# Kernel tuning notes

Hardware: AMD Instinct MI355X
Metric: run time of the kernel (lower is better)

## Reference

```python
import jax, jax.numpy as jnp
import numpy as np
import math

BATCH, SEQ, D_MODEL, HEADS = 2, 2048, 1024, 16
DK = D_MODEL // HEADS  # 64
THETA = 10000.0


def _init_linear(key, d_in, d_out):
    std = math.sqrt(2.0 / (d_in + d_out))
    return (jax.random.truncated_normal(key, -3.0, 3.0, (d_in, d_out), jnp.float32) * std)


def setup_inputs() -> dict:
    key = jax.random.key(0)
    kx, kq, kk, kv, ko = jax.random.split(key, 5)
    x = jax.random.normal(kx, (BATCH, SEQ, D_MODEL), jnp.float32)
    W_Q = _init_linear(kq, D_MODEL, D_MODEL)
    W_K = _init_linear(kk, D_MODEL, D_MODEL)
    W_V = _init_linear(kv, D_MODEL, D_MODEL)
    W_O = _init_linear(ko, D_MODEL, D_MODEL)
    token_positions = jnp.arange(SEQ, dtype=jnp.int64 if jax.config.jax_enable_x64 else jnp.int32)
    # RoPE tables: angle[i, k] = i / theta**(2k/d_k), shape [max_seq_len, d_k//2]
    pos = jnp.arange(SEQ, dtype=jnp.float32)[:, None]
    inv_freq = THETA ** (-2.0 * jnp.arange(DK // 2, dtype=jnp.float32) / DK)
    angles = pos * inv_freq
    return {
        "x": x,
        "token_positions": token_positions,
        "W_Q": W_Q,
        "W_K": W_K,
        "W_V": W_V,
        "W_O": W_O,
        "cos": jnp.cos(angles),
        "sin": jnp.sin(angles),
    }


def _apply_rope(t, cos_p, sin_p):
    # t: [B, H, S, DK]; cos_p/sin_p: [S, DK//2] (already gathered by position)
    t_even = t[..., 0::2]
    t_odd = t[..., 1::2]
    even_rot = cos_p * t_even - sin_p * t_odd
    odd_rot = sin_p * t_even + cos_p * t_odd
    # interleave back: [..., DK//2, 2] -> [..., DK]
    return jnp.stack([even_rot, odd_rot], axis=-1).reshape(t.shape)


def reference(x, token_positions, W_Q, W_K, W_V, W_O, cos, sin):
    B, S, D = x.shape
    H, dk = HEADS, D // HEADS
    # QKV projections, split into heads: [B, S, D] -> [B, H, S, dk]
    def proj(W):
        return jnp.einsum("bsd,de->bse", x, W).reshape(B, S, H, dk).transpose(0, 2, 1, 3)
    Q, K, V = proj(W_Q), proj(W_K), proj(W_V)
    cos_p = cos[token_positions]  # [S, dk//2]
    sin_p = sin[token_positions]
    Q = _apply_rope(Q, cos_p, sin_p)
    K = _apply_rope(K, cos_p, sin_p)
    scores = jnp.einsum("bhqd,bhkd->bhqk", Q, K) / jnp.sqrt(jnp.asarray(dk, x.dtype))
    causal = jnp.tril(jnp.ones((S, S), dtype=bool))
    scores = jnp.where(causal, scores, -jnp.inf)
    attn = jax.nn.softmax(scores, axis=-1)
    out = jnp.einsum("bhqk,bhkd->bhqd", attn, V)  # [B, H, S, dk]
    out = out.transpose(0, 2, 1, 3).reshape(B, S, D)
    return jnp.einsum("bsd,de->bse", out, W_O)
```

## Files before the change

kernel.cpp:

```cpp
#include <hip/hip_runtime.h>

typedef unsigned short u16;
typedef unsigned int   u32;
typedef __bf16  bf16x8 __attribute__((ext_vector_type(8)));
typedef float   f32x4  __attribute__((ext_vector_type(4)));
typedef u32     u32x4  __attribute__((ext_vector_type(4)));

#define SEQ    2048
#define HEADS  16
#define DM     1024
#define NBH    32
#define NBS    4096

#define LOG2E  1.4426950408889634f

__device__ __forceinline__ u16 f2b(float f) {
    u32 x;
    __builtin_memcpy(&x, &f, 4);
    return (u16)((x + 0x7fffu + ((x >> 16) & 1u)) >> 16);
}

__device__ __forceinline__ u32 pkc(float lo, float hi) {
    __bf16 a = (__bf16)lo, b = (__bf16)hi;
    u16 x, y;
    __builtin_memcpy(&x, &a, 2);
    __builtin_memcpy(&y, &b, 2);
    return (u32)x | ((u32)y << 16);
}

__device__ __forceinline__ bf16x8 ld_bf8(const u16* p) {
    return *(const bf16x8*)p;
}

__device__ __forceinline__ void gl_lds16(const u16* g, __bf16* l) {
    __builtin_amdgcn_global_load_lds(
        (__attribute__((address_space(1))) void*)g,
        (__attribute__((address_space(3))) void*)l,
        16, 0, 0);
}

__global__ __launch_bounds__(256) void transpose_wqkv(const float* __restrict__ Wq,
                                                      const float* __restrict__ Wk,
                                                      const float* __restrict__ Wv,
                                                      u16* __restrict__ WqkvT) {
    __shared__ u16 tile[64][65];
    const int z  = blockIdx.z;
    const float* src = (z == 0) ? Wq : (z == 1) ? Wk : Wv;
    const int k0 = blockIdx.x * 64, n0 = blockIdx.y * 64;
    const int tid = threadIdx.x;
    for (int i = 0; i < 16; ++i) {
        int e = i * 256 + tid;
        int r = e >> 6, c = e & 63;
        tile[r][c] = f2b(src[(size_t)(k0 + r) * DM + n0 + c]);
    }
    __syncthreads();
    u16* dst = WqkvT + (size_t)z * DM * DM;
    for (int i = 0; i < 16; ++i) {
        int e = i * 256 + tid;
        int r = e >> 6, c = e & 63;
        dst[(size_t)(n0 + r) * DM + k0 + c] = tile[c][r];
    }
}

__global__ __launch_bounds__(256) void transpose_wo(const float* __restrict__ Wo,
                                                    u16* __restrict__ WoT) {
    __shared__ u16 tile[64][65];
    const int k0 = blockIdx.x * 64, n0 = blockIdx.y * 64;
    const int tid = threadIdx.x;
    for (int i = 0; i < 16; ++i) {
        int e = i * 256 + tid;
        int r = e >> 6, c = e & 63;
        tile[r][c] = f2b(Wo[(size_t)(k0 + r) * DM + n0 + c]);
    }
    __syncthreads();
    for (int i = 0; i < 16; ++i) {
        int e = i * 256 + tid;
        int r = e >> 6, c = e & 63;
        WoT[(size_t)(n0 + r) * DM + k0 + c] = tile[c][r];
    }
}

__global__ __launch_bounds__(256) void cvt_x(const float* __restrict__ x,
                                             u16* __restrict__ xb) {
    int t = blockIdx.x * 256 + threadIdx.x;
    const float* p = x + (size_t)t * 8;
    f32x4 a = *(const f32x4*)p;
    f32x4 b = *(const f32x4*)(p + 4);
    u32x4 v;
    v[0] = pkc(a[0], a[1]);
    v[1] = pkc(a[2], a[3]);
    v[2] = pkc(b[0], b[1]);
    v[3] = pkc(b[2], b[3]);
    *(u32x4*)(xb + (size_t)t * 8) = v;
}

__global__ __launch_bounds__(256) void gemm_qkv(const u16* __restrict__ Ab,
                                                const u16* __restrict__ Bt,
                                                u16* __restrict__ Qp,
                                                u16* __restrict__ Kp,
                                                u16* __restrict__ Vt) {
    __shared__ __attribute__((aligned(16))) __bf16 As[128 * 64];
    __shared__ __attribute__((aligned(16))) __bf16 Bs[128 * 64];
    const int tid  = threadIdx.x;
    const int wave = tid >> 6, lane = tid & 63;
    const int quad = lane >> 4, col = lane & 15;
    const int wm = wave >> 1, wn = wave & 1;
    const int m0 = blockIdx.x * 128, n0 = blockIdx.y * 128;
    const int srow = tid >> 3;
    const int aslot = (((tid & 7) ^ (srow & 7)) << 3);
    const int c7 = col & 7;

    f32x4 zero = {0.f, 0.f, 0.f, 0.f};
    f32x4 acc[4][4];
    for (int i = 0; i < 4; ++i)
        for (int j = 0; j < 4; ++j) acc[i][j] = zero;

    for (int k0 = 0; k0 < DM; k0 += 64) {
        __syncthreads();
#pragma unroll
        for (int p = 0; p < 4; ++p)
            gl_lds16(Ab + (size_t)(m0 + p * 32 + srow) * DM + k0 + aslot,
                     &As[p * 2048 + tid * 8]);
#pragma unroll
        for (int p = 0; p < 4; ++p)
            gl_lds16(Bt + (size_t)(n0 + p * 32 + srow) * DM + k0 + aslot,
                     &Bs[p * 2048 + tid * 8]);
        __syncthreads();
#pragma unroll
        for (int ks = 0; ks < 2; ++ks) {
            const int rsl = ((((ks << 2) | quad) ^ c7) << 3);
            bf16x8 af[4], bfr[4];
#pragma unroll
            for (int mt = 0; mt < 4; ++mt)
                af[mt] = *(const bf16x8*)&As[(wm * 64 + mt * 16 + col) * 64 + rsl];
#pragma unroll
            for (int nt = 0; nt < 4; ++nt)
                bfr[nt] = *(const bf16x8*)&Bs[(wn * 64 + nt * 16 + col) * 64 + rsl];
#pragma unroll
            for (int mt = 0; mt < 4; ++mt)
#pragma unroll
                for (int nt = 0; nt < 4; ++nt)
                    acc[mt][nt] = __builtin_amdgcn_mfma_f32_16x16x32_bf16(
                        af[mt], bfr[nt], acc[mt][nt], 0, 0, 0);
        }
    }

    for (int mt = 0; mt < 4; ++mt)
        for (int nt = 0; nt < 4; ++nt) {
            int cc = n0 + wn * 64 + nt * 16 + col;
            int which = cc >> 10;
            int c1 = cc & 1023;
            int h = c1 >> 6, d = c1 & 63;
            for (int r = 0; r < 4; ++r) {
                int row = m0 + wm * 64 + mt * 16 + quad * 4 + r;
                int b = row >> 11, s = row & (SEQ - 1);
                u16 val = f2b(acc[mt][nt][r]);
                size_t bh = (size_t)(b * HEADS + h);
                if (which == 0)
                    Qp[(bh * SEQ + s) * 64 + d] = val;
                else if (which == 1)
                    Kp[(bh * SEQ + s) * 64 + d] = val;
                else
                    Vt[(bh * 64 + d) * SEQ + s] = val;
            }
        }
}

__global__ __launch_bounds__(256) void gemm_wo(const u16* __restrict__ A,
                                               const u16* __restrict__ Bt,
                                               float* __restrict__ C) {
    __shared__ __attribute__((aligned(16))) __bf16 As[128 * 64];
    __shared__ __attribute__((aligned(16))) __bf16 Bs[64 * 64];
    const int tid  = threadIdx.x;
    const int wave = tid >> 6, lane = tid & 63;
    const int quad = lane >> 4, col = lane & 15;
    const int m0 = blockIdx.x * 128, n0 = blockIdx.y * 64;
    const int srow = tid >> 3;
    const int aslot = (((tid & 7) ^ (srow & 7)) << 3);
    const int c7 = col & 7;

    f32x4 zero = {0.f, 0.f, 0.f, 0.f};
    f32x4 acc[2][4];
    for (int i = 0; i < 2; ++i)
        for (int j = 0; j < 4; ++j) acc[i][j] = zero;

    for (int k0 = 0; k0 < DM; k0 += 64) {
        __syncthreads();
#pragma unroll
        for (int p = 0; p < 4; ++p)
            gl_lds16(A + (size_t)(m0 + p * 32 + srow) * DM + k0 + aslot,
                     &As[p * 2048 + tid * 8]);
#pragma unroll
        for (int p = 0; p < 2; ++p)
            gl_lds16(Bt + (size_t)(n0 + p * 32 + srow) * DM + k0 + aslot,
                     &Bs[p * 2048 + tid * 8]);
        __syncthreads();
#pragma unroll
        for (int ks = 0; ks < 2; ++ks) {
            const int rsl = ((((ks << 2) | quad) ^ c7) << 3);
            bf16x8 af[2], bfr[4];
#pragma unroll
            for (int mt = 0; mt < 2; ++mt)
                af[mt] = *(const bf16x8*)&As[(wave * 32 + mt * 16 + col) * 64 + rsl];
#pragma unroll
            for (int nt = 0; nt < 4; ++nt)
                bfr[nt] = *(const bf16x8*)&Bs[(nt * 16 + col) * 64 + rsl];
#pragma unroll
            for (int mt = 0; mt < 2; ++mt)
#pragma unroll
                for (int nt = 0; nt < 4; ++nt)
                    acc[mt][nt] = __builtin_amdgcn_mfma_f32_16x16x32_bf16(
                        af[mt], bfr[nt], acc[mt][nt], 0, 0, 0);
        }
    }

    for (int mt = 0; mt < 2; ++mt)
        for (int nt = 0; nt < 4; ++nt)
            for (int r = 0; r < 4; ++r) {
                int row = m0 + wave * 32 + mt * 16 + quad * 4 + r;
                int cc  = n0 + nt * 16 + col;
                C[(size_t)row * DM + cc] = acc[mt][nt][r];
            }
}

__global__ __launch_bounds__(256) void rope_qk(u16* __restrict__ Qp,
                                               u16* __restrict__ Kp,
                                               const float* __restrict__ cosT,
                                               const float* __restrict__ sinT) {
    int t = blockIdx.x * 256 + threadIdx.x;
    int g  = t & 7;
    int s  = (t >> 3) & (SEQ - 1);
    int hh = (t >> 14) & (HEADS - 1);
    int b  = t >> 18;

    f32x4 cv = *(const f32x4*)&cosT[s * 32 + g * 4];
    f32x4 sv = *(const f32x4*)&sinT[s * 32 + g * 4];

    const float QS = 0.125f * LOG2E;
    size_t addr = (((size_t)(b * HEADS + hh)) * SEQ + s) * 64 + g * 8;
    u32x4 q4 = *(const u32x4*)(Qp + addr);
    u32x4 k4 = *(const u32x4*)(Kp + addr);
    u32x4 qo4, ko4;
#pragma unroll
    for (int j = 0; j < 4; ++j) {
        u32 q2 = q4[j], k2 = k4[j];
        u32 qe_b = (q2 & 0xffff) << 16, qo_b = q2 & 0xffff0000u;
        u32 ke_b = (k2 & 0xffff) << 16, ko_b = k2 & 0xffff0000u;
        float qe, qo, ke, ko;
        __builtin_memcpy(&qe, &qe_b, 4); __builtin_memcpy(&qo, &qo_b, 4);
        __builtin_memcpy(&ke, &ke_b, 4); __builtin_memcpy(&ko, &ko_b, 4);
        qo4[j] = (u32)f2b(QS * (cv[j] * qe - sv[j] * qo)) |
                 ((u32)f2b(QS * (sv[j] * qe + cv[j] * qo)) << 16);
        ko4[j] = (u32)f2b(cv[j] * ke - sv[j] * ko) |
                 ((u32)f2b(sv[j] * ke + cv[j] * ko) << 16);
    }
    *(u32x4*)(Qp + addr) = qo4;
    *(u32x4*)(Kp + addr) = ko4;
}

__global__ __launch_bounds__(64) void flash_attn(const u16* __restrict__ Qp,
                                                 const u16* __restrict__ Kp,
                                                 const u16* __restrict__ Vt,
                                                 u16* __restrict__ O) {
    const int lane = threadIdx.x;
    const int quad = lane >> 4, col = lane & 15;
    const bool hi5 = lane >= 32;
    const bool hi4 = (lane & 16) != 0;
    const int bh = blockIdx.x;
    const int b = bh >> 4, h = bh & 15;
    const int qt = 63 - blockIdx.y;
    const int q0 = qt * 32;

    const u16* Qb = Qp + (size_t)bh * SEQ * 64;
    const u16* Kb = Kp + (size_t)bh * SEQ * 64;
    const u16* Vb = Vt + (size_t)bh * 64 * SEQ;

    bf16x8 bq00 = ld_bf8(Qb + (size_t)(q0 + col) * 64 + quad * 8);
    bf16x8 bq01 = ld_bf8(Qb + (size_t)(q0 + col) * 64 + 32 + quad * 8);
    bf16x8 bq10 = ld_bf8(Qb + (size_t)(q0 + 16 + col) * 64 + quad * 8);
    bf16x8 bq11 = ld_bf8(Qb + (size_t)(q0 + 16 + col) * 64 + 32 + quad * 8);

    f32x4 zero = {0.f, 0.f, 0.f, 0.f};
    f32x4 o0[4] = {zero, zero, zero, zero};
    f32x4 o1[4] = {zero, zero, zero, zero};
    float m0_ = -1e30f, m1_ = -1e30f;
    float lp0 = 0.f, lp1 = 0.f;

    const int nkt = qt + 1;

    bf16x8 ck00 = ld_bf8(Kb + (size_t)col * 64 + quad * 8);
    bf16x8 ck01 = ld_bf8(Kb + (size_t)col * 64 + 32 + quad * 8);
    bf16x8 ck10 = ld_bf8(Kb + (size_t)(16 + col) * 64 + quad * 8);
    bf16x8 ck11 = ld_bf8(Kb + (size_t)(16 + col) * 64 + 32 + quad * 8);
    bf16x8 cv0  = ld_bf8(Vb + (size_t)(0 * 16 + col) * SEQ + quad * 8);
    bf16x8 cv1  = ld_bf8(Vb + (size_t)(1 * 16 + col) * SEQ + quad * 8);
    bf16x8 cv2  = ld_bf8(Vb + (size_t)(2 * 16 + col) * SEQ + quad * 8);
    bf16x8 cv3  = ld_bf8(Vb + (size_t)(3 * 16 + col) * SEQ + quad * 8);

    for (int kt = 0; kt < nkt; ++kt) {
        const int kb = kt << 5;
        const int kb2 = kb + 32;
        bf16x8 nk00 = ld_bf8(Kb + (size_t)(kb2 + col) * 64 + quad * 8);
        bf16x8 nk01 = ld_bf8(Kb + (size_t)(kb2 + col) * 64 + 32 + quad * 8);
        bf16x8 nk10 = ld_bf8(Kb + (size_t)(kb2 + 16 + col) * 64 + quad * 8);
        bf16x8 nk11 = ld_bf8(Kb + (size_t)(kb2 + 16 + col) * 64 + 32 + quad * 8);
        bf16x8 nv0  = ld_bf8(Vb + (size_t)(0 * 16 + col) * SEQ + kb2 + quad * 8);
        bf16x8 nv1  = ld_bf8(Vb + (size_t)(1 * 16 + col) * SEQ + kb2 + quad * 8);
        bf16x8 nv2  = ld_bf8(Vb + (size_t)(2 * 16 + col) * SEQ + kb2 + quad * 8);
        bf16x8 nv3  = ld_bf8(Vb + (size_t)(3 * 16 + col) * SEQ + kb2 + quad * 8);

        f32x4 s00 = zero, s01 = zero, s10 = zero, s11 = zero;
        s00 = __builtin_amdgcn_mfma_f32_16x16x32_bf16(ck00, bq00, s00, 0, 0, 0);
        s10 = __builtin_amdgcn_mfma_f32_16x16x32_bf16(ck00, bq10, s10, 0, 0, 0);
        s00 = __builtin_amdgcn_mfma_f32_16x16x32_bf16(ck01, bq01, s00, 0, 0, 0);
        s10 = __builtin_amdgcn_mfma_f32_16x16x32_bf16(ck01, bq11, s10, 0, 0, 0);
        s01 = __builtin_amdgcn_mfma_f32_16x16x32_bf16(ck10, bq00, s01, 0, 0, 0);
        s11 = __builtin_amdgcn_mfma_f32_16x16x32_bf16(ck10, bq10, s11, 0, 0, 0);
        s01 = __builtin_amdgcn_mfma_f32_16x16x32_bf16(ck11, bq01, s01, 0, 0, 0);
        s11 = __builtin_amdgcn_mfma_f32_16x16x32_bf16(ck11, bq11, s11, 0, 0, 0);

        float v00[4], v01[4], v10[4], v11[4];
        float lm0 = -1e30f, lm1 = -1e30f;
        if (kt == qt) {
            for (int r = 0; r < 4; ++r) {
                int krel = quad * 4 + r;
                float a0 = (krel > col) ? -1e30f : s00[r];
                float b0 = -1e30f;
                float a1 = s10[r];
                float b1 = (krel > col) ? -1e30f : s11[r];
                v00[r] = a0; v01[r] = b0; v10[r] = a1; v11[r] = b1;
                lm0 = fmaxf(lm0, fmaxf(a0, b0));
                lm1 = fmaxf(lm1, fmaxf(a1, b1));
            }
        } else {
            for (int r = 0; r < 4; ++r) {
                v00[r] = s00[r]; v01[r] = s01[r];
                v10[r] = s10[r]; v11[r] = s11[r];
                lm0 = fmaxf(lm0, fmaxf(v00[r], v01[r]));
                lm1 = fmaxf(lm1, fmaxf(v10[r], v11[r]));
            }
        }

        float dd = fmaxf(lm0 - m0_, lm1 - m1_);
        if (__any(dd > 11.54f)) {
            float lr0 = fmaxf(lm0, __shfl_xor(lm0, 16));
            lr0 = fmaxf(lr0, __shfl_xor(lr0, 32));
            float lr1 = fmaxf(lm1, __shfl_xor(lm1, 16));
            lr1 = fmaxf(lr1, __shfl_xor(lr1, 32));
            float mn0 = fmaxf(m0_, lr0), mn1 = fmaxf(m1_, lr1);
            float al0 = __builtin_amdgcn_exp2f(m0_ - mn0);
            float al1 = __builtin_amdgcn_exp2f(m1_ - mn1);
            m0_ = mn0; m1_ = mn1;
            lp0 *= al0; lp1 *= al1;
            for (int r = 0; r < 4; ++r) {
                float ar0 = __shfl(al0, quad * 4 + r);
                float ar1 = __shfl(al1, quad * 4 + r);
                for (int nt = 0; nt < 4; ++nt) {
                    o0[nt][r] *= ar0;
                    o1[nt][r] *= ar1;
                }
            }
        }

        for (int r = 0; r < 4; ++r) {
            v00[r] = __builtin_amdgcn_exp2f(v00[r] - m0_);
            v01[r] = __builtin_amdgcn_exp2f(v01[r] - m0_);
            v10[r] = __builtin_amdgcn_exp2f(v10[r] - m1_);
            v11[r] = __builtin_amdgcn_exp2f(v11[r] - m1_);
            lp0 += v00[r] + v01[r];
            lp1 += v10[r] + v11[r];
        }

        u32 fwa0[4], fwa1[4];
        {
            u32 A0 = pkc(v00[0], v00[1]), A1 = pkc(v00[2], v00[3]);
            u32 B0 = pkc(v01[0], v01[1]), B1 = pkc(v01[2], v01[3]);
            u32 g0 = hi5 ? A0 : B0,  g1 = hi5 ? A1 : B1;
            u32 r0 = __shfl_xor(g0, 32), r1 = __shfl_xor(g1, 32);
            u32 P00 = hi5 ? r0 : A0,  P01 = hi5 ? r1 : A1;
            u32 P10 = hi5 ? B0 : r0,  P11 = hi5 ? B1 : r1;
            u32 h0 = hi4 ? P00 : P10, h1 = hi4 ? P01 : P11;
            u32 u0 = __shfl_xor(h0, 16), u1 = __shfl_xor(h1, 16);
            fwa0[0] = hi4 ? u0 : P00;  fwa0[1] = hi4 ? u1 : P01;
            fwa0[2] = hi4 ? P10 : u0;  fwa0[3] = hi4 ? P11 : u1;
        }
        {
            u32 A0 = pkc(v10[0], v10[1]), A1 = pkc(v10[2], v10[3]);
            u32 B0 = pkc(v11[0], v11[1]), B1 = pkc(v11[2], v11[3]);
            u32 g0 = hi5 ? A0 : B0,  g1 = hi5 ? A1 : B1;
            u32 r0 = __shfl_xor(g0, 32), r1 = __shfl_xor(g1, 32);
            u32 P00 = hi5 ? r0 : A0,  P01 = hi5 ? r1 : A1;
            u32 P10 = hi5 ? B0 : r0,  P11 = hi5 ? B1 : r1;
            u32 h0 = hi4 ? P00 : P10, h1 = hi4 ? P01 : P11;
            u32 u0 = __shfl_xor(h0, 16), u1 = __shfl_xor(h1, 16);
            fwa1[0] = hi4 ? u0 : P00;  fwa1[1] = hi4 ? u1 : P01;
            fwa1[2] = hi4 ? P10 : u0;  fwa1[3] = hi4 ? P11 : u1;
        }
        bf16x8 pf0, pf1;
        __builtin_memcpy(&pf0, fwa0, 16);
        __builtin_memcpy(&pf1, fwa1, 16);

        o0[0] = __builtin_amdgcn_mfma_f32_16x16x32_bf16(pf0, cv0, o0[0], 0, 0, 0);
        o1[0] = __builtin_amdgcn_mfma_f32_16x16x32_bf16(pf1, cv0, o1[0], 0, 0, 0);
        o0[1] = __builtin_amdgcn_mfma_f32_16x16x32_bf16(pf0, cv1, o0[1], 0, 0, 0);
        o1[1] = __builtin_amdgcn_mfma_f32_16x16x32_bf16(pf1, cv1, o1[1], 0, 0, 0);
        o0[2] = __builtin_amdgcn_mfma_f32_16x16x32_bf16(pf0, cv2, o0[2], 0, 0, 0);
        o1[2] = __builtin_amdgcn_mfma_f32_16x16x32_bf16(pf1, cv2, o1[2], 0, 0, 0);
        o0[3] = __builtin_amdgcn_mfma_f32_16x16x32_bf16(pf0, cv3, o0[3], 0, 0, 0);
        o1[3] = __builtin_amdgcn_mfma_f32_16x16x32_bf16(pf1, cv3, o1[3], 0, 0, 0);

        ck00 = nk00; ck01 = nk01; ck10 = nk10; ck11 = nk11;
        cv0 = nv0; cv1 = nv1; cv2 = nv2; cv3 = nv3;
    }

    float lt0 = lp0;
    lt0 += __shfl_xor(lt0, 16); lt0 += __shfl_xor(lt0, 32);
    float lt1 = lp1;
    lt1 += __shfl_xor(lt1, 16); lt1 += __shfl_xor(lt1, 32);
    float linv0 = 1.f / lt0;
    float linv1 = 1.f / lt1;
    for (int r = 0; r < 4; ++r) {
        float l0r = __shfl(linv0, quad * 4 + r);
        float l1r = __shfl(linv1, quad * 4 + r);
        int qrA = q0 + quad * 4 + r;
        int qrB = qrA + 16;
        for (int nt = 0; nt < 4; ++nt) {
            O[((size_t)b * SEQ + qrA) * DM + h * 64 + nt * 16 + col] =
                f2b(o0[nt][r] * l0r);
            O[((size_t)b * SEQ + qrB) * DM + h * 64 + nt * 16 + col] =
                f2b(o1[nt][r] * l1r);
        }
    }
}

extern "C" void kernel_launch(void* const* d_in, const int* in_sizes, int n_in,
                              void* d_out, int out_size, void* d_ws, size_t ws_size,
                              hipStream_t stream) {
    const float* x    = (const float*)d_in[0];
    const float* Wq   = (const float*)d_in[2];
    const float* Wk   = (const float*)d_in[3];
    const float* Wv   = (const float*)d_in[4];
    const float* Wo   = (const float*)d_in[5];
    const float* cosT = (const float*)d_in[6];
    const float* sinT = (const float*)d_in[7];
    float* out = (float*)d_out;

    u16* ws    = (u16*)d_ws;
    u16* qp    = ws;
    u16* kp    = ws + 4194304;
    u16* vt    = ws + 8388608;
    u16* woT   = ws + 8388608;
    u16* wqkvT = ws + 12582912;
    u16* ao    = ws + 12582912;
    u16* xb    = (u16*)out;

    dim3 blk(256);
    transpose_wqkv<<<dim3(16, 16, 3), blk, 0, stream>>>(Wq, Wk, Wv, wqkvT);
    cvt_x<<<dim3(2048), blk, 0, stream>>>(x, xb);
    gemm_qkv<<<dim3(32, 24), blk, 0, stream>>>(xb, wqkvT, qp, kp, vt);
    rope_qk<<<dim3(2048), blk, 0, stream>>>(qp, kp, cosT, sinT);
    flash_attn<<<dim3(NBH, 64), dim3(64), 0, stream>>>(qp, kp, vt, ao);
    transpose_wo<<<dim3(16, 16), blk, 0, stream>>>(Wo, woT);
    gemm_wo<<<dim3(32, 16), blk, 0, stream>>>(ao, woT, out);
}
```

Measured before the change: 238.0 us.

## Split causal KV loop across two waves per block and merge via LDS

The flash attention block grows from one wave to two. Each wave handles alternating 32-key tiles and keeps its own running max, sum and output. At the end, wave 1 writes its partial state to shared memory and wave 0 rescales and combines the two before writing the output. The loop now keeps two tiles of K/V in flight per wave, aiming to shorten each block's serial chain and hide more memory and exp latency. The cost is extra shared memory, a block-level barrier, a merge step and more registers per wave.

```diff
diff --git a/kernel.cpp b/kernel.cpp
--- a/kernel.cpp
+++ b/kernel.cpp
@@ -258,11 +258,118 @@
     *(u32x4*)(Kp + addr) = ko4;
 }
 
-__global__ __launch_bounds__(64) void flash_attn(const u16* __restrict__ Qp,
-                                                 const u16* __restrict__ Kp,
-                                                 const u16* __restrict__ Vt,
-                                                 u16* __restrict__ O) {
-    const int lane = threadIdx.x;
+#define FA_MFMA(A, B, C) __builtin_amdgcn_mfma_f32_16x16x32_bf16(A, B, C, 0, 0, 0)
+
+#define FA_LD(K00, K01, K10, K11, V0, V1, V2, V3, T) do {                      \
+    size_t kk_ = (size_t)(T) * 2048;                                           \
+    size_t vv_ = (size_t)(T) * 32;                                             \
+    K00 = ld_bf8(Kb + kk_ + koff);                                             \
+    K01 = ld_bf8(Kb + kk_ + koff + 32);                                        \
+    K10 = ld_bf8(Kb + kk_ + koff + 1024);                                      \
+    K11 = ld_bf8(Kb + kk_ + koff + 1056);                                      \
+    V0  = ld_bf8(Vb + vv_ + voff);                                             \
+    V1  = ld_bf8(Vb + vv_ + voff + 16 * SEQ);                                  \
+    V2  = ld_bf8(Vb + vv_ + voff + 32 * SEQ);                                  \
+    V3  = ld_bf8(Vb + vv_ + voff + 48 * SEQ);                                  \
+} while (0)
+
+#define FA_TILE(K00, K01, K10, K11, V0, V1, V2, V3, KT) do {                   \
+    f32x4 s00 = zero, s01 = zero, s10 = zero, s11 = zero;                      \
+    s00 = FA_MFMA(K00, bq00, s00);  s10 = FA_MFMA(K00, bq10, s10);             \
+    s00 = FA_MFMA(K01, bq01, s00);  s10 = FA_MFMA(K01, bq11, s10);             \
+    s01 = FA_MFMA(K10, bq00, s01);  s11 = FA_MFMA(K10, bq10, s11);             \
+    s01 = FA_MFMA(K11, bq01, s01);  s11 = FA_MFMA(K11, bq11, s11);             \
+    float v00[4], v01[4], v10[4], v11[4];                                      \
+    float lm0 = -1e30f, lm1 = -1e30f;                                          \
+    if ((KT) == qt) {                        \
+        for (int r = 0; r < 4; ++r) {                                          \
+            int krel = quad * 4 + r;                                           \
+            float a0 = (krel > col) ? -1e30f : s00[r];                         \
+            float b0 = -1e30f;                                                 \
+            float a1 = s10[r];                                                 \
+            float b1 = (krel > col) ? -1e30f : s11[r];                         \
+            v00[r] = a0; v01[r] = b0; v10[r] = a1; v11[r] = b1;                \
+            lm0 = fmaxf(lm0, fmaxf(a0, b0));                                   \
+            lm1 = fmaxf(lm1, fmaxf(a1, b1));                                   \
+        }                                                                      \
+    } else {                                                                   \
+        for (int r = 0; r < 4; ++r) {                                          \
+            v00[r] = s00[r]; v01[r] = s01[r];                                  \
+            v10[r] = s10[r]; v11[r] = s11[r];                                  \
+            lm0 = fmaxf(lm0, fmaxf(v00[r], v01[r]));                           \
+            lm1 = fmaxf(lm1, fmaxf(v10[r], v11[r]));                           \
+        }                                                                      \
+    }                                                                          \
+    float dd = fmaxf(lm0 - m0_, lm1 - m1_);                                    \
+    if (__any(dd > 11.54f)) {                     \
+        float lr0 = fmaxf(lm0, __shfl_xor(lm0, 16));                           \
+        lr0 = fmaxf(lr0, __shfl_xor(lr0, 32));                                 \
+        float lr1 = fmaxf(lm1, __shfl_xor(lm1, 16));                           \
+        lr1 = fmaxf(lr1, __shfl_xor(lr1, 32));                                 \
+        float mn0 = fmaxf(m0_, lr0), mn1 = fmaxf(m1_, lr1);                    \
+        float al0 = __builtin_amdgcn_exp2f(m0_ - mn0);                         \
+        float al1 = __builtin_amdgcn_exp2f(m1_ - mn1);                         \
+        m0_ = mn0; m1_ = mn1;                                                  \
+        lp0 *= al0; lp1 *= al1;                                                \
+        for (int r = 0; r < 4; ++r) {                                          \
+            float ar0 = __shfl(al0, quad * 4 + r);                             \
+            float ar1 = __shfl(al1, quad * 4 + r);                             \
+            for (int nt = 0; nt < 4; ++nt) {                                   \
+                o0[nt][r] *= ar0;                                              \
+                o1[nt][r] *= ar1;                                              \
+            }                                                                  \
+        }                                                                      \
+    }                                                                          \
+    for (int r = 0; r < 4; ++r) {                                              \
+        v00[r] = __builtin_amdgcn_exp2f(v00[r] - m0_);                         \
+        v01[r] = __builtin_amdgcn_exp2f(v01[r] - m0_);                         \
+        v10[r] = __builtin_amdgcn_exp2f(v10[r] - m1_);                         \
+        v11[r] = __builtin_amdgcn_exp2f(v11[r] - m1_);                         \
+        lp0 += v00[r] + v01[r];                                                \
+        lp1 += v10[r] + v11[r];                                                \
+    }                                                                          \
+    u32 fwa0[4], fwa1[4];                                                      \
+    {                                                                          \
+        u32 A0 = pkc(v00[0], v00[1]), A1 = pkc(v00[2], v00[3]);                \
+        u32 B0 = pkc(v01[0], v01[1]), B1 = pkc(v01[2], v01[3]);                \
+        u32 g0 = hi5 ? A0 : B0,  g1 = hi5 ? A1 : B1;                           \
+        u32 r0 = __shfl_xor(g0, 32), r1 = __shfl_xor(g1, 32);                  \
+        u32 P00 = hi5 ? r0 : A0,  P01 = hi5 ? r1 : A1;                         \
+        u32 P10 = hi5 ? B0 : r0,  P11 = hi5 ? B1 : r1;                         \
+        u32 h0 = hi4 ? P00 : P10, h1 = hi4 ? P01 : P11;                        \
+        u32 u0 = __shfl_xor(h0, 16), u1 = __shfl_xor(h1, 16);                  \
+        fwa0[0] = hi4 ? u0 : P00;  fwa0[1] = hi4 ? u1 : P01;                   \
+        fwa0[2] = hi4 ? P10 : u0;  fwa0[3] = hi4 ? P11 : u1;                   \
+    }                                                                          \
+    {                                                                          \
+        u32 A0 = pkc(v10[0], v10[1]), A1 = pkc(v10[2], v10[3]);                \
+        u32 B0 = pkc(v11[0], v11[1]), B1 = pkc(v11[2], v11[3]);                \
+        u32 g0 = hi5 ? A0 : B0,  g1 = hi5 ? A1 : B1;                           \
+        u32 r0 = __shfl_xor(g0, 32), r1 = __shfl_xor(g1, 32);                  \
+        u32 P00 = hi5 ? r0 : A0,  P01 = hi5 ? r1 : A1;                         \
+        u32 P10 = hi5 ? B0 : r0,  P11 = hi5 ? B1 : r1;                         \
+        u32 h0 = hi4 ? P00 : P10, h1 = hi4 ? P01 : P11;                        \
+        u32 u0 = __shfl_xor(h0, 16), u1 = __shfl_xor(h1, 16);                  \
+        fwa1[0] = hi4 ? u0 : P00;  fwa1[1] = hi4 ? u1 : P01;                   \
+        fwa1[2] = hi4 ? P10 : u0;  fwa1[3] = hi4 ? P11 : u1;                   \
+    }                                                                          \
+    bf16x8 pf0, pf1;                                                           \
+    __builtin_memcpy(&pf0, fwa0, 16);                                          \
+    __builtin_memcpy(&pf1, fwa1, 16);                                          \
+    o0[0] = FA_MFMA(pf0, V0, o0[0]);  o1[0] = FA_MFMA(pf1, V0, o1[0]);         \
+    o0[1] = FA_MFMA(pf0, V1, o0[1]);  o1[1] = FA_MFMA(pf1, V1, o1[1]);         \
+    o0[2] = FA_MFMA(pf0, V2, o0[2]);  o1[2] = FA_MFMA(pf1, V2, o1[2]);         \
+    o0[3] = FA_MFMA(pf0, V3, o0[3]);  o1[3] = FA_MFMA(pf1, V3, o1[3]);         \
+} while (0)
+
+__global__ __launch_bounds__(128) void flash_attn(const u16* __restrict__ Qp,
+                                                  const u16* __restrict__ Kp,
+                                                  const u16* __restrict__ Vt,
+                                                  u16* __restrict__ O) {
+    __shared__ float osm[32][68];
+    __shared__ float mMm[32], mLm[32];
+    const int tid  = threadIdx.x;
+    const int wave = tid >> 6, lane = tid & 63;
     const int quad = lane >> 4, col = lane & 15;
     const bool hi5 = lane >= 32;
     const bool hi4 = (lane & 16) != 0;
@@ -287,148 +394,70 @@
     float lp0 = 0.f, lp1 = 0.f;
 
     const int nkt = qt + 1;
-
-    bf16x8 ck00 = ld_bf8(Kb + (size_t)col * 64 + quad * 8);
-    bf16x8 ck01 = ld_bf8(Kb + (size_t)col * 64 + 32 + quad * 8);
-    bf16x8 ck10 = ld_bf8(Kb + (size_t)(16 + col) * 64 + quad * 8);
-    bf16x8 ck11 = ld_bf8(Kb + (size_t)(16 + col) * 64 + 32 + quad * 8);
-    bf16x8 cv0  = ld_bf8(Vb + (size_t)(0 * 16 + col) * SEQ + quad * 8);
-    bf16x8 cv1  = ld_bf8(Vb + (size_t)(1 * 16 + col) * SEQ + quad * 8);
-    bf16x8 cv2  = ld_bf8(Vb + (size_t)(2 * 16 + col) * SEQ + quad * 8);
-    bf16x8 cv3  = ld_bf8(Vb + (size_t)(3 * 16 + col) * SEQ + quad * 8);
-
-    for (int kt = 0; kt < nkt; ++kt) {
-        const int kb = kt << 5;
-        const int kb2 = kb + 32;
-        bf16x8 nk00 = ld_bf8(Kb + (size_t)(kb2 + col) * 64 + quad * 8);
-        bf16x8 nk01 = ld_bf8(Kb + (size_t)(kb2 + col) * 64 + 32 + quad * 8);
-        bf16x8 nk10 = ld_bf8(Kb + (size_t)(kb2 + 16 + col) * 64 + quad * 8);
-        bf16x8 nk11 = ld_bf8(Kb + (size_t)(kb2 + 16 + col) * 64 + 32 + quad * 8);
-        bf16x8 nv0  = ld_bf8(Vb + (size_t)(0 * 16 + col) * SEQ + kb2 + quad * 8);
-        bf16x8 nv1  = ld_bf8(Vb + (size_t)(1 * 16 + col) * SEQ + kb2 + quad * 8);
-        bf16x8 nv2  = ld_bf8(Vb + (size_t)(2 * 16 + col) * SEQ + kb2 + quad * 8);
-        bf16x8 nv3  = ld_bf8(Vb + (size_t)(3 * 16 + col) * SEQ + kb2 + quad * 8);
-
-        f32x4 s00 = zero, s01 = zero, s10 = zero, s11 = zero;
-        s00 = __builtin_amdgcn_mfma_f32_16x16x32_bf16(ck00, bq00, s00, 0, 0, 0);
-        s10 = __builtin_amdgcn_mfma_f32_16x16x32_bf16(ck00, bq10, s10, 0, 0, 0);
-        s00 = __builtin_amdgcn_mfma_f32_16x16x32_bf16(ck01, bq01, s00, 0, 0, 0);
-        s10 = __builtin_amdgcn_mfma_f32_16x16x32_bf16(ck01, bq11, s10, 0, 0, 0);
-        s01 = __builtin_amdgcn_mfma_f32_16x16x32_bf16(ck10, bq00, s01, 0, 0, 0);
-        s11 = __builtin_amdgcn_mfma_f32_16x16x32_bf16(ck10, bq10, s11, 0, 0, 0);
-        s01 = __builtin_amdgcn_mfma_f32_16x16x32_bf16(ck11, bq01, s01, 0, 0, 0);
-        s11 = __builtin_amdgcn_mfma_f32_16x16x32_bf16(ck11, bq11, s11, 0, 0, 0);
-
-        float v00[4], v01[4], v10[4], v11[4];
-        float lm0 = -1e30f, lm1 = -1e30f;
-        if (kt == qt) {
-            for (int r = 0; r < 4; ++r) {
-                int krel = quad * 4 + r;
-                float a0 = (krel > col) ? -1e30f : s00[r];
-                float b0 = -1e30f;
-                float a1 = s10[r];
-                float b1 = (krel > col) ? -1e30f : s11[r];
-                v00[r] = a0; v01[r] = b0; v10[r] = a1; v11[r] = b1;
-                lm0 = fmaxf(lm0, fmaxf(a0, b0));
-                lm1 = fmaxf(lm1, fmaxf(a1, b1));
-            }
-        } else {
-            for (int r = 0; r < 4; ++r) {
-                v00[r] = s00[r]; v01[r] = s01[r];
-                v10[r] = s10[r]; v11[r] = s11[r];
-                lm0 = fmaxf(lm0, fmaxf(v00[r], v01[r]));
-                lm1 = fmaxf(lm1, fmaxf(v10[r], v11[r]));
-            }
-        }
-
-        float dd = fmaxf(lm0 - m0_, lm1 - m1_);
-        if (__any(dd > 11.54f)) {
-            float lr0 = fmaxf(lm0, __shfl_xor(lm0, 16));
-            lr0 = fmaxf(lr0, __shfl_xor(lr0, 32));
-            float lr1 = fmaxf(lm1, __shfl_xor(lm1, 16));
-            lr1 = fmaxf(lr1, __shfl_xor(lr1, 32));
-            float mn0 = fmaxf(m0_, lr0), mn1 = fmaxf(m1_, lr1);
-            float al0 = __builtin_amdgcn_exp2f(m0_ - mn0);
-            float al1 = __builtin_amdgcn_exp2f(m1_ - mn1);
-            m0_ = mn0; m1_ = mn1;
-            lp0 *= al0; lp1 *= al1;
-            for (int r = 0; r < 4; ++r) {
-                float ar0 = __shfl(al0, quad * 4 + r);
-                float ar1 = __shfl(al1, quad * 4 + r);
-                for (int nt = 0; nt < 4; ++nt) {
-                    o0[nt][r] *= ar0;
-                    o1[nt][r] *= ar1;
-                }
-            }
-        }
-
-        for (int r = 0; r < 4; ++r) {
-            v00[r] = __builtin_amdgcn_exp2f(v00[r] - m0_);
-            v01[r] = __builtin_amdgcn_exp2f(v01[r] - m0_);
-            v10[r] = __builtin_amdgcn_exp2f(v10[r] - m1_);
-            v11[r] = __builtin_amdgcn_exp2f(v11[r] - m1_);
-            lp0 += v00[r] + v01[r];
-            lp1 += v10[r] + v11[r];
-        }
-
-        u32 fwa0[4], fwa1[4];
-        {
-            u32 A0 = pkc(v00[0], v00[1]), A1 = pkc(v00[2], v00[3]);
-            u32 B0 = pkc(v01[0], v01[1]), B1 = pkc(v01[2], v01[3]);
-            u32 g0 = hi5 ? A0 : B0,  g1 = hi5 ? A1 : B1;
-            u32 r0 = __shfl_xor(g0, 32), r1 = __shfl_xor(g1, 32);
-            u32 P00 = hi5 ? r0 : A0,  P01 = hi5 ? r1 : A1;
-            u32 P10 = hi5 ? B0 : r0,  P11 = hi5 ? B1 : r1;
-            u32 h0 = hi4 ? P00 : P10, h1 = hi4 ? P01 : P11;
-            u32 u0 = __shfl_xor(h0, 16), u1 = __shfl_xor(h1, 16);
-            fwa0[0] = hi4 ? u0 : P00;  fwa0[1] = hi4 ? u1 : P01;
-            fwa0[2] = hi4 ? P10 : u0;  fwa0[3] = hi4 ? P11 : u1;
-        }
-        {
-            u32 A0 = pkc(v10[0], v10[1]), A1 = pkc(v10[2], v10[3]);
-            u32 B0 = pkc(v11[0], v11[1]), B1 = pkc(v11[2], v11[3]);
-            u32 g0 = hi5 ? A0 : B0,  g1 = hi5 ? A1 : B1;
-            u32 r0 = __shfl_xor(g0, 32), r1 = __shfl_xor(g1, 32);
-            u32 P00 = hi5 ? r0 : A0,  P01 = hi5 ? r1 : A1;
-            u32 P10 = hi5 ? B0 : r0,  P11 = hi5 ? B1 : r1;
-            u32 h0 = hi4 ? P00 : P10, h1 = hi4 ? P01 : P11;
-            u32 u0 = __shfl_xor(h0, 16), u1 = __shfl_xor(h1, 16);
-            fwa1[0] = hi4 ? u0 : P00;  fwa1[1] = hi4 ? u1 : P01;
-            fwa1[2] = hi4 ? P10 : u0;  fwa1[3] = hi4 ? P11 : u1;
-        }
-        bf16x8 pf0, pf1;
-        __builtin_memcpy(&pf0, fwa0, 16);
-        __builtin_memcpy(&pf1, fwa1, 16);
-
-        o0[0] = __builtin_amdgcn_mfma_f32_16x16x32_bf16(pf0, cv0, o0[0], 0, 0, 0);
-        o1[0] = __builtin_amdgcn_mfma_f32_16x16x32_bf16(pf1, cv0, o1[0], 0, 0, 0);
-        o0[1] = __builtin_amdgcn_mfma_f32_16x16x32_bf16(pf0, cv1, o0[1], 0, 0, 0);
-        o1[1] = __builtin_amdgcn_mfma_f32_16x16x32_bf16(pf1, cv1, o1[1], 0, 0, 0);
-        o0[2] = __builtin_amdgcn_mfma_f32_16x16x32_bf16(pf0, cv2, o0[2], 0, 0, 0);
-        o1[2] = __builtin_amdgcn_mfma_f32_16x16x32_bf16(pf1, cv2, o1[2], 0, 0, 0);
-        o0[3] = __builtin_amdgcn_mfma_f32_16x16x32_bf16(pf0, cv3, o0[3], 0, 0, 0);
-        o1[3] = __builtin_amdgcn_mfma_f32_16x16x32_bf16(pf1, cv3, o1[3], 0, 0, 0);
-
-        ck00 = nk00; ck01 = nk01; ck10 = nk10; ck11 = nk11;
-        cv0 = nv0; cv1 = nv1; cv2 = nv2; cv3 = nv3;
+    const size_t koff = (size_t)col * 64 + quad * 8;
+    const size_t voff = (size_t)col * SEQ + quad * 8;
+
+    int kt = wave;
+    if (kt < nkt) {
+        bf16x8 aK00, aK01, aK10, aK11, aV0, aV1, aV2, aV3;
+        bf16x8 cK00, cK01, cK10, cK11, cV0, cV1, cV2, cV3;
+        FA_LD(aK00, aK01, aK10, aK11, aV0, aV1, aV2, aV3, kt);
+        FA_LD(cK00, cK01, cK10, cK11, cV0, cV1, cV2, cV3, kt + 2);
+        while (true) {
+            FA_TILE(aK00, aK01, aK10, aK11, aV0, aV1, aV2, aV3, kt);
+            kt += 2; if (kt >= nkt) break;
+            FA_LD(aK00, aK01, aK10, aK11, aV0, aV1, aV2, aV3, kt + 2);
+            FA_TILE(cK00, cK01, cK10, cK11, cV0, cV1, cV2, cV3, kt);
+            kt += 2; if (kt >= nkt) break;
+            FA_LD(cK00, cK01, cK10, cK11, cV0, cV1, cV2, cV3, kt + 2);
+        }
     }
 
     float lt0 = lp0;
     lt0 += __shfl_xor(lt0, 16); lt0 += __shfl_xor(lt0, 32);
     float lt1 = lp1;
     lt1 += __shfl_xor(lt1, 16); lt1 += __shfl_xor(lt1, 32);
-    float linv0 = 1.f / lt0;
-    float linv1 = 1.f / lt1;
-    for (int r = 0; r < 4; ++r) {
-        float l0r = __shfl(linv0, quad * 4 + r);
-        float l1r = __shfl(linv1, quad * 4 + r);
-        int qrA = q0 + quad * 4 + r;
-        int qrB = qrA + 16;
-        for (int nt = 0; nt < 4; ++nt) {
-            O[((size_t)b * SEQ + qrA) * DM + h * 64 + nt * 16 + col] =
-                f2b(o0[nt][r] * l0r);
-            O[((size_t)b * SEQ + qrB) * DM + h * 64 + nt * 16 + col] =
-                f2b(o1[nt][r] * l1r);
+
+    if (wave == 1) {
+        if (quad == 0) {
+            mMm[col] = m0_;      mLm[col] = lt0;
+            mMm[16 + col] = m1_; mLm[16 + col] = lt1;
+        }
+        for (int nt = 0; nt < 4; ++nt)
+            for (int r = 0; r < 4; ++r) {
+                osm[quad * 4 + r][nt * 16 + col]      = o0[nt][r];
+                osm[16 + quad * 4 + r][nt * 16 + col] = o1[nt][r];
+            }
+    }
+    __syncthreads();
+
+    if (wave == 0) {
+        for (int r = 0; r < 4; ++r) {
+            const int qr = quad * 4 + r;
+            {
+                float mw0 = __shfl(m0_, qr);
+                float lw0 = __shfl(lt0, qr);
+                float mw1 = mMm[qr], lw1 = mLm[qr];
+                float M  = fmaxf(mw0, mw1);
+                float e0 = __builtin_amdgcn_exp2f(mw0 - M);
+                float e1 = __builtin_amdgcn_exp2f(mw1 - M);
+                float inv = 1.f / (e0 * lw0 + e1 * lw1);
+                for (int nt = 0; nt < 4; ++nt)
+                    O[((size_t)b * SEQ + q0 + qr) * DM + h * 64 + nt * 16 + col] =
+                        f2b((e0 * o0[nt][r] + e1 * osm[qr][nt * 16 + col]) * inv);
+            }
+            {
+                float mw0 = __shfl(m1_, qr);
+                float lw0 = __shfl(lt1, qr);
+                float mw1 = mMm[16 + qr], lw1 = mLm[16 + qr];
+                float M  = fmaxf(mw0, mw1);
+                float e0 = __builtin_amdgcn_exp2f(mw0 - M);
+                float e1 = __builtin_amdgcn_exp2f(mw1 - M);
+                float inv = 1.f / (e0 * lw0 + e1 * lw1);
+                for (int nt = 0; nt < 4; ++nt)
+                    O[((size_t)b * SEQ + q0 + 16 + qr) * DM + h * 64 + nt * 16 + col] =
+                        f2b((e0 * o1[nt][r] + e1 * osm[16 + qr][nt * 16 + col]) * inv);
+            }
         }
     }
 }
@@ -459,7 +488,7 @@
     cvt_x<<<dim3(2048), blk, 0, stream>>>(x, xb);
     gemm_qkv<<<dim3(32, 24), blk, 0, stream>>>(xb, wqkvT, qp, kp, vt);
     rope_qk<<<dim3(2048), blk, 0, stream>>>(qp, kp, cosT, sinT);
-    flash_attn<<<dim3(NBH, 64), dim3(64), 0, stream>>>(qp, kp, vt, ao);
+    flash_attn<<<dim3(NBH, 64), dim3(128), 0, stream>>>(qp, kp, vt, ao);
     transpose_wo<<<dim3(16, 16), blk, 0, stream>>>(Wo, woT);
     gemm_wo<<<dim3(32, 16), blk, 0, stream>>>(ao, woT, out);
 }
```

Measured after the change: 233.6 us. No clear change (-1.8%).
